# Kernel optimization log

Measured on AMD Instinct MI355X. Metric: run time of the kernel, lower is better.

The kernel has to match this reference:

```python
import jax, jax.numpy as jnp
import numpy as np

D_MODEL = 1024
N_HEADS = 16
HEAD_DIM = D_MODEL // N_HEADS
SEQ_LEN = 2048
BATCH = 2
THETA = 10000.0


def _rope_tables(dim, seq_len, theta=THETA):
    freqs = 1.0 / theta ** (jnp.arange(0, dim, 2, dtype=jnp.float32) / dim)  # (dim/2,)
    t = jnp.arange(seq_len, dtype=jnp.float32)
    ang = jnp.outer(t, freqs)  # (S, dim/2)
    # interleave each freq twice to match the (-x_odd, x_even) rotation layout
    cos = jnp.repeat(jnp.cos(ang), 2, axis=-1)  # (S, dim)
    sin = jnp.repeat(jnp.sin(ang), 2, axis=-1)
    return cos, sin


def _apply_rope(x, cos, sin):
    # x: (B, S, H, D); cos/sin: (S, D)
    x_rot = jnp.stack([-x[..., 1::2], x[..., ::2]], axis=-1).reshape(x.shape)
    return x * cos[None, :, None, :] + x_rot * sin[None, :, None, :]


def setup_inputs() -> dict:
    key = jax.random.key(0)
    ks = jax.random.split(key, 9)
    s = 1.0 / np.sqrt(D_MODEL)
    return {
        "x": jax.random.normal(ks[0], (BATCH, SEQ_LEN, D_MODEL), dtype=jnp.float32),
        "wq": jax.random.normal(ks[1], (D_MODEL, D_MODEL), jnp.float32) * s,
        "bq": jnp.zeros((D_MODEL,), jnp.float32),
        "wk": jax.random.normal(ks[2], (D_MODEL, D_MODEL), jnp.float32) * s,
        "bk": jnp.zeros((D_MODEL,), jnp.float32),
        "wv": jax.random.normal(ks[3], (D_MODEL, D_MODEL), jnp.float32) * s,
        "bv": jnp.zeros((D_MODEL,), jnp.float32),
        "wo": jax.random.normal(ks[4], (D_MODEL, D_MODEL), jnp.float32) * s,
        "bo": jnp.zeros((D_MODEL,), jnp.float32),
    }


def reference(x, wq, bq, wk, bk, wv, bv, wo, bo):
    B, S, _ = x.shape
    cos, sin = _rope_tables(HEAD_DIM, S)
    # projections (torch Linear: x @ W^T + b)
    q = (x @ wq.T + bq).reshape(B, S, N_HEADS, HEAD_DIM)
    k = (x @ wk.T + bk).reshape(B, S, N_HEADS, HEAD_DIM)
    v = (x @ wv.T + bv).reshape(B, S, N_HEADS, HEAD_DIM)
    q = _apply_rope(q, cos, sin)
    k = _apply_rope(k, cos, sin)
    # attention: bhqd, bhkd -> bhqk
    scale = 1.0 / np.sqrt(HEAD_DIM)
    scores = jnp.einsum("bqhd,bkhd->bhqk", q, k) * scale
    attn = jax.nn.softmax(scores, axis=-1)
    out = jnp.einsum("bhqk,bkhd->bqhd", attn, v).reshape(B, S, D_MODEL)
    return out @ wo.T + bo
```

## Files before the change

kernel.cpp:

```cpp
#include <hip/hip_runtime.h>

typedef __attribute__((ext_vector_type(8))) __bf16 bf16x8;
typedef __attribute__((ext_vector_type(4))) float f32x4;
typedef __attribute__((ext_vector_type(4))) unsigned short ushort4v;

__device__ __forceinline__ unsigned short f2bf(float f) {
  unsigned u = __builtin_bit_cast(unsigned, f);
  u += 0x7fffu + ((u >> 16) & 1u);
  return (unsigned short)(u >> 16);
}

__device__ __forceinline__ void gload16(const void* g, void* l) {
  __builtin_amdgcn_global_load_lds(
      (const __attribute__((address_space(1))) void*)g,
      (__attribute__((address_space(3))) void*)l, 16, 0, 0);
}

__global__ __launch_bounds__(256) void rope_tab_k(float* cosT, float* sinT) {
  const int idx = blockIdx.x * 256 + threadIdx.x;
  const int s = idx >> 5, j = idx & 31;
  const float freq = powf(10000.f, -(float)(2 * j) * (1.f / 64.f));
  const float ang = (float)s * freq;
  cosT[idx] = cosf(ang);
  sinT[idx] = sinf(ang);
}

__global__ __launch_bounds__(256) void convert_k(
    const float* __restrict__ x, const float* __restrict__ wq,
    const float* __restrict__ wk, const float* __restrict__ wv,
    const float* __restrict__ wo,
    unsigned short* __restrict__ xb, unsigned short* __restrict__ wqkv,
    unsigned short* __restrict__ wob) {
  const size_t i = ((size_t)blockIdx.x * 256 + threadIdx.x) * 4;
  const float* src; unsigned short* dst; size_t off;
  if (i < 4194304)      { src = x;  dst = xb;              off = i; }
  else if (i < 5242880) { src = wq; dst = wqkv;            off = i - 4194304; }
  else if (i < 6291456) { src = wk; dst = wqkv + 1048576;  off = i - 5242880; }
  else if (i < 7340032) { src = wv; dst = wqkv + 2097152;  off = i - 6291456; }
  else                  { src = wo; dst = wob;             off = i - 7340032; }
  f32x4 v = *(const f32x4*)(src + off);
  ushort4v o;
  o[0] = f2bf(v[0]); o[1] = f2bf(v[1]); o[2] = f2bf(v[2]); o[3] = f2bf(v[3]);
  *(ushort4v*)(dst + off) = o;
}

template <int EPI>
__global__ __launch_bounds__(256) void gemm_bt_k(
    const unsigned short* __restrict__ A, const unsigned short* __restrict__ B,
    int M, int N, int K,
    unsigned short* __restrict__ Qr, unsigned short* __restrict__ Kr,
    unsigned short* __restrict__ Vt,
    const float* __restrict__ bq, const float* __restrict__ bk,
    const float* __restrict__ bvv,
    const float* __restrict__ cosT, const float* __restrict__ sinT,
    float* __restrict__ Cout, const float* __restrict__ bias) {
  __shared__ char smem[32768];
  const int t = threadIdx.x;
  const int wave = t >> 6, lane = t & 63;
  const int l15 = lane & 15, g = lane >> 4;
  const int nt = N >> 7;
  const int mb = (blockIdx.x / nt) << 7;
  const int nb = (blockIdx.x % nt) << 7;
  const int wm = (wave >> 1) << 6;
  const int wn = (wave & 1) << 6;

  const f32x4 zv = {0.f, 0.f, 0.f, 0.f};
  f32x4 acc[4][4];
#pragma unroll
  for (int i = 0; i < 4; i++)
#pragma unroll
    for (int j = 0; j < 4; j++) acc[i][j] = zv;

  for (int kt = 0; kt < K; kt += 64) {
#pragma unroll
    for (int i = 0; i < 4; i++) {
      const int lin = t * 16 + i * 4096;
      const int r = lin >> 7;
      const int cb = (lin & 127) ^ ((r & 7) << 4);
      gload16((const char*)A + ((size_t)(mb + r) * K + kt) * 2 + cb,
              smem + i * 4096 + wave * 1024);
      gload16((const char*)B + ((size_t)(nb + r) * K + kt) * 2 + cb,
              smem + 16384 + i * 4096 + wave * 1024);
    }
    __syncthreads();

    bf16x8 af[4][2], bfr[4][2];
    const int sw = (l15 & 7) << 4;
#pragma unroll
    for (int mf = 0; mf < 4; mf++) {
      const int r = wm + mf * 16 + l15;
      const int r2 = wn + mf * 16 + l15;
#pragma unroll
      for (int kf = 0; kf < 2; kf++) {
        af[mf][kf]  = *(const bf16x8*)(smem + r * 128 + ((kf * 64 + g * 16) ^ sw));
        bfr[mf][kf] = *(const bf16x8*)(smem + 16384 + r2 * 128 + ((kf * 64 + g * 16) ^ sw));
      }
    }
#pragma unroll
    for (int mf = 0; mf < 4; mf++)
#pragma unroll
      for (int nf = 0; nf < 4; nf++) {
        acc[mf][nf] = __builtin_amdgcn_mfma_f32_16x16x32_bf16(af[mf][0], bfr[nf][0], acc[mf][nf], 0, 0, 0);
        acc[mf][nf] = __builtin_amdgcn_mfma_f32_16x16x32_bf16(af[mf][1], bfr[nf][1], acc[mf][nf], 0, 0, 0);
      }
    __syncthreads();
  }

#pragma unroll
  for (int mf = 0; mf < 4; mf++) {
#pragma unroll
    for (int nf = 0; nf < 4; nf++) {
      const int row0 = mb + wm + mf * 16 + g * 4;
      const int col = nb + wn + nf * 16 + l15;
      if (EPI == 1) {
        const float bsv = bias[col];
#pragma unroll
        for (int r = 0; r < 4; r++)
          Cout[(size_t)(row0 + r) * N + col] = acc[mf][nf][r] + bsv;
      } else {
        const int region = col >> 10;
        const int cc = col & 1023;
        const int h = cc >> 6, d = cc & 63;
        const float bias_v = (region == 0 ? bq : (region == 1 ? bk : bvv))[cc];
        if (region < 2) {
          unsigned short* Ob = (region == 0 ? Qr : Kr);
          const float scl = (region == 0) ? 0.180336880111120425f : 1.0f;
#pragma unroll
          for (int r = 0; r < 4; r++) {
            const int row = row0 + r;
            const int s = row & 2047;
            const int b = row >> 11;
            const float v = acc[mf][nf][r] + bias_v;
            const float p = __shfl_xor(v, 1);
            const float c = cosT[s * 32 + (d >> 1)];
            const float sn = sinT[s * 32 + (d >> 1)];
            float o = (d & 1) ? (v * c + p * sn) : (v * c - p * sn);
            o *= scl;
            Ob[((size_t)(b * 16 + h) * 2048 + s) * 64 + d] = f2bf(o);
          }
        } else {
          ushort4v w;
#pragma unroll
          for (int r = 0; r < 4; r++) w[r] = f2bf(acc[mf][nf][r] + bias_v);
          const int s = row0 & 2047;
          const int b = row0 >> 11;
          *(ushort4v*)(Vt + ((size_t)(b * 16 + h) * 64 + d) * 2048 + s) = w;
        }
      }
    }
  }
}

__global__ __launch_bounds__(512, 4) void flash_k(
    const unsigned short* __restrict__ Qr, const unsigned short* __restrict__ Kr,
    const unsigned short* __restrict__ Vt, unsigned short* __restrict__ Oa) {
  __shared__ char smem[49152];
  const int bid = blockIdx.x;
  const int wi = bid >> 3;
  const int bh = ((bid & 7) << 2) | (wi & 3);
  const int qt = wi >> 2;
  const int t = threadIdx.x;
  const int wave = t >> 6, lane = t & 63;
  const int l15 = lane & 15, g = lane >> 4;
  char* pbuf = smem + 32768 + wave * 2048;
  const int q0 = qt * 128 + wave * 16;
  const unsigned short* Qb = Qr + ((size_t)bh * 2048 + q0) * 64;
  const char* Kb = (const char*)(Kr + (size_t)bh * 2048 * 64);
  const char* Vb = (const char*)(Vt + (size_t)bh * 64 * 2048);

  const int srow = t >> 3;
  const int scb = ((t & 7) * 16) ^ ((srow & 7) << 4);

  const bf16x8 qf0 = *(const bf16x8*)(Qb + l15 * 64 + g * 8);
  const bf16x8 qf1 = *(const bf16x8*)(Qb + l15 * 64 + g * 8 + 32);

  const f32x4 zv = {0.f, 0.f, 0.f, 0.f};
  f32x4 ot[4];
#pragma unroll
  for (int i = 0; i < 4; i++) ot[i] = zv;
  float m = -1e30f, lsum = 0.f;
  const int sw = (l15 & 7) << 4;

  {
    gload16(Kb + (size_t)srow * 128 + scb, smem + wave * 1024);
    gload16(Vb + (size_t)srow * 4096 + scb, smem + 8192 + wave * 1024);
  }
  __syncthreads();

  for (int it = 0; it < 32; ++it) {
    const int cur = it & 1;
    const char* kb = smem + cur * 16384;
    const char* vb = kb + 8192;
    if (it < 31) {
      const int kvn = (it + 1) << 6;
      char* kd = smem + (cur ^ 1) * 16384;
      gload16(Kb + (size_t)(kvn + srow) * 128 + scb, kd + wave * 1024);
      gload16(Vb + (size_t)srow * 4096 + kvn * 2 + scb, kd + 8192 + wave * 1024);
    }
    f32x4 st[4];
#pragma unroll
    for (int s = 0; s < 4; s++) {
      const int rb = (s * 16 + l15) * 128;
      const bf16x8 k0 = *(const bf16x8*)(kb + rb + ((g * 16) ^ sw));
      const bf16x8 k1 = *(const bf16x8*)(kb + rb + ((64 + g * 16) ^ sw));
      f32x4 a = __builtin_amdgcn_mfma_f32_16x16x32_bf16(k0, qf0, zv, 0, 0, 0);
      st[s] = __builtin_amdgcn_mfma_f32_16x16x32_bf16(k1, qf1, a, 0, 0, 0);
    }
    float tmax = st[0][0];
#pragma unroll
    for (int s = 0; s < 4; s++)
#pragma unroll
      for (int e = 0; e < 4; e++) tmax = fmaxf(tmax, st[s][e]);
    tmax = fmaxf(tmax, __shfl_xor(tmax, 16));
    tmax = fmaxf(tmax, __shfl_xor(tmax, 32));
    if (!__all(tmax <= m + 8.0f)) {
      const float mn = fmaxf(m, tmax);
      const float al = __builtin_amdgcn_exp2f(m - mn);
      lsum *= al;
#pragma unroll
      for (int i = 0; i < 4; i++) {
        ot[i][0] *= al; ot[i][1] *= al; ot[i][2] *= al; ot[i][3] *= al;
      }
      m = mn;
    }
#pragma unroll
    for (int s = 0; s < 4; s++)
#pragma unroll
      for (int e = 0; e < 4; e++) {
        const float p = __builtin_amdgcn_exp2f(st[s][e] - m);
        st[s][e] = p;
        lsum += p;
      }
#pragma unroll
    for (int s = 0; s < 4; s++) {
      ushort4v w;
#pragma unroll
      for (int e = 0; e < 4; e++) w[e] = f2bf(st[s][e]);
      *(ushort4v*)(pbuf + ((l15 * 128 + s * 32 + g * 8) ^ sw)) = w;
    }
    asm volatile("" ::: "memory");
#pragma unroll
    for (int h = 0; h < 2; h++) {
      const bf16x8 pb = *(const bf16x8*)(pbuf + ((l15 * 128 + h * 64 + g * 16) ^ sw));
#pragma unroll
      for (int dc = 0; dc < 4; dc++) {
        const bf16x8 va = *(const bf16x8*)(vb + (dc * 16 + l15) * 128 + ((h * 64 + g * 16) ^ sw));
        ot[dc] = __builtin_amdgcn_mfma_f32_16x16x32_bf16(va, pb, ot[dc], 0, 0, 0);
      }
    }
    __syncthreads();
  }
  lsum += __shfl_xor(lsum, 16);
  lsum += __shfl_xor(lsum, 32);
  const float inv = 1.f / lsum;
  const int b = bh >> 4, h = bh & 15;
  const size_t rowbase = ((size_t)(b * 2048 + q0 + l15)) * 1024 + h * 64;
#pragma unroll
  for (int dc = 0; dc < 4; dc++) {
    ushort4v w;
#pragma unroll
    for (int r = 0; r < 4; r++) w[r] = f2bf(ot[dc][r] * inv);
    *(ushort4v*)(Oa + rowbase + dc * 16 + g * 4) = w;
  }
}

extern "C" void kernel_launch(void* const* d_in, const int* in_sizes, int n_in,
                              void* d_out, int out_size, void* d_ws, size_t ws_size,
                              hipStream_t stream) {
  const float* x  = (const float*)d_in[0];
  const float* wq = (const float*)d_in[1];
  const float* bq = (const float*)d_in[2];
  const float* wk = (const float*)d_in[3];
  const float* bk = (const float*)d_in[4];
  const float* wv = (const float*)d_in[5];
  const float* bv = (const float*)d_in[6];
  const float* wo = (const float*)d_in[7];
  const float* bo = (const float*)d_in[8];
  float* out = (float*)d_out;
  char* ws = (char*)d_ws;

  unsigned short* xb   = (unsigned short*)(ws);
  unsigned short* wqkv = (unsigned short*)(ws + 8388608);
  unsigned short* wob  = (unsigned short*)(ws + 14680064);
  float* cosT          = (float*)(ws + 16777216);
  float* sinT          = (float*)(ws + 17039360);
  unsigned short* Qr   = (unsigned short*)(ws + 17301504);
  unsigned short* Kr   = (unsigned short*)(ws + 25690112);
  unsigned short* Vt   = (unsigned short*)(ws + 34078720);
  unsigned short* Oa   = (unsigned short*)(ws + 42467328);

  rope_tab_k<<<dim3(256), dim3(256), 0, stream>>>(cosT, sinT);
  convert_k<<<dim3(8192), dim3(256), 0, stream>>>(x, wq, wk, wv, wo, xb, wqkv, wob);
  gemm_bt_k<0><<<dim3(32 * 24), dim3(256), 0, stream>>>(
      xb, wqkv, 4096, 3072, 1024, Qr, Kr, Vt, bq, bk, bv, cosT, sinT,
      (float*)nullptr, (const float*)nullptr);
  flash_k<<<dim3(512), dim3(512), 0, stream>>>(Qr, Kr, Vt, Oa);
  gemm_bt_k<1><<<dim3(32 * 8), dim3(256), 0, stream>>>(
      Oa, wob, 4096, 1024, 1024,
      (unsigned short*)nullptr, (unsigned short*)nullptr, (unsigned short*)nullptr,
      (const float*)nullptr, (const float*)nullptr, (const float*)nullptr,
      cosT, sinT, out, bo);
}
```

Measured before the change: 138.2 us.

## Shrink flash blocks to four waves, fuse RoPE table into convert kernel

The flash attention kernel now launches 1024 blocks of 256 threads, each handling 64 query rows, and each thread issues two async K/V tile loads instead of one. Shared memory per block drops to 40 KB. This gives more, smaller blocks to fill the CUs and reduces per-block LDS pressure, but each K/V tile is now loaded by twice as many blocks. The RoPE table kernel is merged into convert_k as extra blocks to save a launch, the softmax row sum uses split partial accumulators, and bf16 conversion uses native casts.

```diff
diff --git a/kernel.cpp b/kernel.cpp
--- a/kernel.cpp
+++ b/kernel.cpp
@@ -1,6 +1,7 @@
 #include <hip/hip_runtime.h>
 
 typedef __attribute__((ext_vector_type(8))) __bf16 bf16x8;
+typedef __attribute__((ext_vector_type(4))) __bf16 bf16x4;
 typedef __attribute__((ext_vector_type(4))) float f32x4;
 typedef __attribute__((ext_vector_type(4))) unsigned short ushort4v;
 
@@ -14,15 +15,6 @@
   __builtin_amdgcn_global_load_lds(
       (const __attribute__((address_space(1))) void*)g,
       (__attribute__((address_space(3))) void*)l, 16, 0, 0);
-}
-
-__global__ __launch_bounds__(256) void rope_tab_k(float* cosT, float* sinT) {
-  const int idx = blockIdx.x * 256 + threadIdx.x;
-  const int s = idx >> 5, j = idx & 31;
-  const float freq = powf(10000.f, -(float)(2 * j) * (1.f / 64.f));
-  const float ang = (float)s * freq;
-  cosT[idx] = cosf(ang);
-  sinT[idx] = sinf(ang);
 }
 
 __global__ __launch_bounds__(256) void convert_k(
@@ -30,7 +22,16 @@
     const float* __restrict__ wk, const float* __restrict__ wv,
     const float* __restrict__ wo,
     unsigned short* __restrict__ xb, unsigned short* __restrict__ wqkv,
-    unsigned short* __restrict__ wob) {
+    unsigned short* __restrict__ wob, float* cosT, float* sinT) {
+  if (blockIdx.x >= 8192) {
+    const int idx = (blockIdx.x - 8192) * 256 + threadIdx.x;
+    const int s = idx >> 5, j = idx & 31;
+    const float freq = powf(10000.f, -(float)(2 * j) * (1.f / 64.f));
+    const float ang = (float)s * freq;
+    cosT[idx] = cosf(ang);
+    sinT[idx] = sinf(ang);
+    return;
+  }
   const size_t i = ((size_t)blockIdx.x * 256 + threadIdx.x) * 4;
   const float* src; unsigned short* dst; size_t off;
   if (i < 4194304)      { src = x;  dst = xb;              off = i; }
@@ -151,26 +152,22 @@
   }
 }
 
-__global__ __launch_bounds__(512, 4) void flash_k(
+__global__ __launch_bounds__(256, 4) void flash_k(
     const unsigned short* __restrict__ Qr, const unsigned short* __restrict__ Kr,
     const unsigned short* __restrict__ Vt, unsigned short* __restrict__ Oa) {
-  __shared__ char smem[49152];
+  __shared__ char smem[40960];
   const int bid = blockIdx.x;
-  const int wi = bid >> 3;
-  const int bh = ((bid & 7) << 2) | (wi & 3);
-  const int qt = wi >> 2;
+  const int bh = ((bid & 7) << 2) | ((bid >> 3) & 3);
+  const int qt = bid >> 5;
   const int t = threadIdx.x;
   const int wave = t >> 6, lane = t & 63;
   const int l15 = lane & 15, g = lane >> 4;
   char* pbuf = smem + 32768 + wave * 2048;
-  const int q0 = qt * 128 + wave * 16;
+  const int q0 = qt * 64 + wave * 16;
   const unsigned short* Qb = Qr + ((size_t)bh * 2048 + q0) * 64;
   const char* Kb = (const char*)(Kr + (size_t)bh * 2048 * 64);
   const char* Vb = (const char*)(Vt + (size_t)bh * 64 * 2048);
 
-  const int srow = t >> 3;
-  const int scb = ((t & 7) * 16) ^ ((srow & 7) << 4);
-
   const bf16x8 qf0 = *(const bf16x8*)(Qb + l15 * 64 + g * 8);
   const bf16x8 qf1 = *(const bf16x8*)(Qb + l15 * 64 + g * 8 + 32);
 
@@ -181,9 +178,13 @@
   float m = -1e30f, lsum = 0.f;
   const int sw = (l15 & 7) << 4;
 
-  {
-    gload16(Kb + (size_t)srow * 128 + scb, smem + wave * 1024);
-    gload16(Vb + (size_t)srow * 4096 + scb, smem + 8192 + wave * 1024);
+#pragma unroll
+  for (int i = 0; i < 2; i++) {
+    const int lin = t * 16 + i * 4096;
+    const int r = lin >> 7;
+    const int cb = (lin & 127) ^ ((r & 7) << 4);
+    gload16(Kb + (size_t)r * 128 + cb, smem + i * 4096 + wave * 1024);
+    gload16(Vb + (size_t)r * 4096 + cb, smem + 8192 + i * 4096 + wave * 1024);
   }
   __syncthreads();
 
@@ -194,8 +195,14 @@
     if (it < 31) {
       const int kvn = (it + 1) << 6;
       char* kd = smem + (cur ^ 1) * 16384;
-      gload16(Kb + (size_t)(kvn + srow) * 128 + scb, kd + wave * 1024);
-      gload16(Vb + (size_t)srow * 4096 + kvn * 2 + scb, kd + 8192 + wave * 1024);
+#pragma unroll
+      for (int i = 0; i < 2; i++) {
+        const int lin = t * 16 + i * 4096;
+        const int r = lin >> 7;
+        const int cb = (lin & 127) ^ ((r & 7) << 4);
+        gload16(Kb + (size_t)(kvn + r) * 128 + cb, kd + i * 4096 + wave * 1024);
+        gload16(Vb + (size_t)r * 4096 + kvn * 2 + cb, kd + 8192 + i * 4096 + wave * 1024);
+      }
     }
     f32x4 st[4];
 #pragma unroll
@@ -223,20 +230,24 @@
       }
       m = mn;
     }
-#pragma unroll
-    for (int s = 0; s < 4; s++)
+    float ls[4];
+#pragma unroll
+    for (int s = 0; s < 4; s++) {
+      ls[s] = 0.f;
 #pragma unroll
       for (int e = 0; e < 4; e++) {
         const float p = __builtin_amdgcn_exp2f(st[s][e] - m);
         st[s][e] = p;
-        lsum += p;
-      }
+        ls[s] += p;
+      }
+    }
+    lsum += (ls[0] + ls[1]) + (ls[2] + ls[3]);
 #pragma unroll
     for (int s = 0; s < 4; s++) {
-      ushort4v w;
-#pragma unroll
-      for (int e = 0; e < 4; e++) w[e] = f2bf(st[s][e]);
-      *(ushort4v*)(pbuf + ((l15 * 128 + s * 32 + g * 8) ^ sw)) = w;
+      bf16x4 w;
+#pragma unroll
+      for (int e = 0; e < 4; e++) w[e] = (__bf16)st[s][e];
+      *(bf16x4*)(pbuf + ((l15 * 128 + s * 32 + g * 8) ^ sw)) = w;
     }
     asm volatile("" ::: "memory");
 #pragma unroll
@@ -257,10 +268,10 @@
   const size_t rowbase = ((size_t)(b * 2048 + q0 + l15)) * 1024 + h * 64;
 #pragma unroll
   for (int dc = 0; dc < 4; dc++) {
-    ushort4v w;
-#pragma unroll
-    for (int r = 0; r < 4; r++) w[r] = f2bf(ot[dc][r] * inv);
-    *(ushort4v*)(Oa + rowbase + dc * 16 + g * 4) = w;
+    bf16x4 w;
+#pragma unroll
+    for (int r = 0; r < 4; r++) w[r] = (__bf16)(ot[dc][r] * inv);
+    *(bf16x4*)(Oa + rowbase + dc * 16 + g * 4) = w;
   }
 }
 
@@ -289,12 +300,11 @@
   unsigned short* Vt   = (unsigned short*)(ws + 34078720);
   unsigned short* Oa   = (unsigned short*)(ws + 42467328);
 
-  rope_tab_k<<<dim3(256), dim3(256), 0, stream>>>(cosT, sinT);
-  convert_k<<<dim3(8192), dim3(256), 0, stream>>>(x, wq, wk, wv, wo, xb, wqkv, wob);
+  convert_k<<<dim3(8448), dim3(256), 0, stream>>>(x, wq, wk, wv, wo, xb, wqkv, wob, cosT, sinT);
   gemm_bt_k<0><<<dim3(32 * 24), dim3(256), 0, stream>>>(
       xb, wqkv, 4096, 3072, 1024, Qr, Kr, Vt, bq, bk, bv, cosT, sinT,
       (float*)nullptr, (const float*)nullptr);
-  flash_k<<<dim3(512), dim3(512), 0, stream>>>(Qr, Kr, Vt, Oa);
+  flash_k<<<dim3(1024), dim3(256), 0, stream>>>(Qr, Kr, Vt, Oa);
   gemm_bt_k<1><<<dim3(32 * 8), dim3(256), 0, stream>>>(
       Oa, wob, 4096, 1024, 1024,
       (unsigned short*)nullptr, (unsigned short*)nullptr, (unsigned short*)nullptr,
```

New measurement: 136.8 us. No clear change (-0.9%).
